# Performance work log

Measured on AMD Instinct MI355X. Metric: run time of the kernel, lower is better.

Reference implementation:

```python
import jax, jax.numpy as jnp
import numpy as np

N_NODES = 100000
FIELD_DIM = 128
EMBED_DIM = 64
N_EDGES = 3200000
BATCH = 8192
NUM_FIELDS = 2


def setup_inputs() -> dict:
    key = jax.random.key(0)
    k1, k2, k3, k4 = jax.random.split(key, 4)
    features = jax.random.normal(k1, (N_NODES, FIELD_DIM), dtype=jnp.float32)
    edge_index = jax.random.randint(k2, (2, N_EDGES), 0, N_NODES, dtype=jnp.int32)
    # GCNConv linear weight (Glorot-ish scale) and bias
    W = jax.random.normal(k3, (FIELD_DIM, EMBED_DIM), dtype=jnp.float32) * (1.0 / np.sqrt(FIELD_DIM))
    bias = jnp.zeros((EMBED_DIM,), dtype=jnp.float32)
    x = jax.random.randint(k4, (BATCH, NUM_FIELDS), 0, N_NODES, dtype=jnp.int32)
    return {"features": features, "edge_index": edge_index, "W": W, "bias": bias, "x": x}


def reference(features, edge_index, W, bias, x):
    # GCNConv: out = D^{-1/2} (A + I) D^{-1/2} (X W) + b, then gather rows by x.
    n = features.shape[0]
    loop = jnp.arange(n, dtype=edge_index.dtype)
    src = jnp.concatenate([edge_index[0], loop])  # [E + N]
    dst = jnp.concatenate([edge_index[1], loop])  # [E + N]
    # degree (with self-loops) per destination node; >= 1 so rsqrt is safe
    deg = jax.ops.segment_sum(jnp.ones_like(dst, dtype=features.dtype), dst, num_segments=n)
    dinv = jax.lax.rsqrt(deg)
    norm = dinv[src] * dinv[dst]  # [E + N]
    h = features @ W  # [N, EMBED_DIM]
    msgs = h[src] * norm[:, None]  # gather + scale
    out = jax.ops.segment_sum(msgs, dst, num_segments=n) + bias  # [N, EMBED_DIM]
    return out[x]  # [BATCH, NUM_FIELDS, EMBED_DIM]
```

## Files before the change

### kernel.cpp

```cpp
#include <hip/hip_runtime.h>

#define N_NODES   100000
#define FIELD_DIM 128
#define EMBED_DIM 64
#define N_EDGES   3200000
#define NX        16384

#define NRANGE    2
#define RN        50000
#define RNH       25000
#define NSLICE    125
#define SLICE_E   (N_EDGES / NSLICE)
#define HISTB     (NRANGE * NSLICE)
#define SB_N      16384
#define EXB       (N_EDGES / 1024)
#define GEMMB     ((N_NODES + 63) / 64)
#define EGB       (EXB + GEMMB)
#define PCAP      5120

typedef short  bf16x8 __attribute__((ext_vector_type(8)));
typedef float  f32x4  __attribute__((ext_vector_type(4)));

__device__ __forceinline__ unsigned short f2bf(float x) {
    unsigned u = __float_as_uint(x);
    u += 0x7FFF + ((u >> 16) & 1);
    return (unsigned short)(u >> 16);
}
__device__ __forceinline__ float bf2f(unsigned short b) {
    return __uint_as_float(((unsigned)b) << 16);
}
__device__ __forceinline__ unsigned pk2(float lo, float hi) {
    return (unsigned)f2bf(lo) | ((unsigned)f2bf(hi) << 16);
}

__global__ __launch_bounds__(1024) void k_histzero(const int* __restrict__ dst,
                                                   unsigned int* __restrict__ partial32,
                                                   float4* __restrict__ z4) {
    int tid = threadIdx.x;
    if (blockIdx.x == HISTB) {
        for (int i = tid; i < 1284; i += 1024) z4[i] = make_float4(0.f, 0.f, 0.f, 0.f);
        return;
    }
    __shared__ unsigned int hist[RNH];
    int q = blockIdx.x & 1, s = blockIdx.x >> 1;
    for (int i = tid; i < RNH; i += 1024) hist[i] = 0;
    __syncthreads();
    int lo = q * RN;
    const int4* dp = (const int4*)(dst + s * SLICE_E);
    for (int i = tid; i < SLICE_E / 4; i += 1024) {
        int4 d = dp[i];
        int a;
        a = d.x - lo; if ((unsigned)a < RN) atomicAdd(&hist[a >> 1], 1u << ((a & 1) << 4));
        a = d.y - lo; if ((unsigned)a < RN) atomicAdd(&hist[a >> 1], 1u << ((a & 1) << 4));
        a = d.z - lo; if ((unsigned)a < RN) atomicAdd(&hist[a >> 1], 1u << ((a & 1) << 4));
        a = d.w - lo; if ((unsigned)a < RN) atomicAdd(&hist[a >> 1], 1u << ((a & 1) << 4));
    }
    __syncthreads();
    unsigned int* po = partial32 + (size_t)blockIdx.x * RNH;
    for (int i = tid; i < RNH; i += 1024) po[i] = hist[i];
}

__global__ void k_init(const int* __restrict__ x, unsigned int* __restrict__ bits,
                       const float* __restrict__ W, unsigned short* __restrict__ Wt) {
    int b = blockIdx.x;
    if (b < 64) {
        int i = b * 256 + threadIdx.x;
        int v = x[i];
        atomicOr(&bits[v >> 5], 1u << (v & 31));
    } else {
        for (int o = threadIdx.x; o < FIELD_DIM * EMBED_DIM; o += 256) {
            int c = o >> 7, k = o & 127;
            Wt[o] = f2bf(W[k * EMBED_DIM + c]);
        }
    }
}

__global__ __launch_bounds__(256) void k_reduce(const unsigned int* __restrict__ partial32,
                                                const unsigned int* __restrict__ bits,
                                                int* __restrict__ cnt,
                                                float* __restrict__ dinv,
                                                int* __restrict__ nlist,
                                                int* __restrict__ inv,
                                                int* __restrict__ off,
                                                int* __restrict__ sbase_t,
                                                unsigned long long* __restrict__ counters) {
    __shared__ int wtot[4], wedge[4], ptot[4], pedge[4];
    __shared__ unsigned int baseN, baseE;
    int tid = threadIdx.x;
    int v = blockIdx.x * 256 + tid;
    bool inb = (v < N_NODES);
    int vc = inb ? v : (N_NODES - 1);
    int q = vc / RN, loc = vc - q * RN;
    int i2 = loc >> 1, sh = (loc & 1) << 4;
    const unsigned int* p = partial32 + (size_t)q * RNH + i2;
    unsigned short vals[NSLICE];
#pragma unroll
    for (int s = 0; s < NSLICE; ++s)
        vals[s] = (unsigned short)((p[(size_t)s * (NRANGE * RNH)] >> sh) & 0xFFFFu);
    int c = 0;
#pragma unroll
    for (int s = 0; s < NSLICE; ++s) c += vals[s];
    if (inb) {
        cnt[v] = c;
        dinv[v] = rsqrtf((float)c + 1.0f);
    }
    bool fl = inb && ((bits[v >> 5] >> (v & 31)) & 1u);
    int lane = tid & 63;
    int w = tid >> 6;
    unsigned long long mask = __ballot(fl);
    int cc = fl ? c : 0;
    int incl = cc;
#pragma unroll
    for (int o = 1; o < 64; o <<= 1) {
        int t = __shfl_up(incl, o);
        if (lane >= o) incl += t;
    }
    if (lane == 63) { wtot[w] = __popcll(mask); wedge[w] = incl; }
    int myi = __popcll(mask & ((1ull << lane) - 1));
    int excl = incl - cc;
    __syncthreads();
    if (tid == 0) {
        int t0 = wtot[0], t1 = wtot[1], t2 = wtot[2], t3 = wtot[3];
        int e0 = wedge[0], e1 = wedge[1], e2 = wedge[2], e3 = wedge[3];
        ptot[0] = 0; ptot[1] = t0; ptot[2] = t0 + t1; ptot[3] = t0 + t1 + t2;
        pedge[0] = 0; pedge[1] = e0; pedge[2] = e0 + e1; pedge[3] = e0 + e1 + e2;
        int bt = t0 + t1 + t2 + t3;
        int be = e0 + e1 + e2 + e3;
        if (bt > 0) {
            unsigned long long add = ((unsigned long long)(unsigned)be << 32) |
                                     (unsigned long long)(unsigned)bt;
            unsigned long long old = atomicAdd(counters, add);
            baseN = (unsigned)(old & 0xFFFFFFFFull);
            baseE = (unsigned)(old >> 32);
        } else {
            baseN = 0; baseE = 0;
        }
    }
    __syncthreads();
    if (fl) {
        int ic = (int)baseN + ptot[w] + myi;
        int oc = (int)baseE + pedge[w] + excl;
        nlist[ic] = v;
        inv[v] = ic;
        off[v] = oc;
        int cum = 0;
#pragma unroll
        for (int s = 0; s < NSLICE; ++s) {
            sbase_t[(size_t)s * SB_N + ic] = oc + cum;
            cum += vals[s];
        }
    }
}

__global__ __launch_bounds__(256) void k_exgemm(const int* __restrict__ src,
                                                const int* __restrict__ dst,
                                                const unsigned int* __restrict__ bits,
                                                const int* __restrict__ inv,
                                                int2* __restrict__ pairs,
                                                int* __restrict__ scur16,
                                                const float* __restrict__ F,
                                                const unsigned short* __restrict__ Wt,
                                                unsigned short* __restrict__ h) {
    int bk = blockIdx.x;
    int tid = threadIdx.x;
    bool isg = ((bk % 3) == 0) && (bk / 3 < GEMMB);
    if (!isg) {
        __shared__ int wsum[4];
        __shared__ int sbase;
        int b = bk - min(bk / 3 + 1, GEMMB);
        int lane = tid & 63, w = tid >> 6;
        int slice = b / 25;
        const int4* dp = (const int4*)(dst + b * 1024);
        const int4* sp = (const int4*)(src + b * 1024);
        int4 d4 = dp[tid];
        int4 s4 = sp[tid];
        int dd[4] = {d4.x, d4.y, d4.z, d4.w};
        int ss[4] = {s4.x, s4.y, s4.z, s4.w};
        bool fl[4];
        int nf = 0;
#pragma unroll
        for (int u = 0; u < 4; ++u) {
            fl[u] = (bits[(unsigned)dd[u] >> 5] >> (dd[u] & 31)) & 1u;
            nf += fl[u] ? 1 : 0;
        }
        int incl = nf;
#pragma unroll
        for (int o = 1; o < 64; o <<= 1) {
            int t = __shfl_up(incl, o);
            if (lane >= o) incl += t;
        }
        if (lane == 63) wsum[w] = incl;
        __syncthreads();
        if (tid == 0) {
            int bt = wsum[0] + wsum[1] + wsum[2] + wsum[3];
            sbase = bt ? atomicAdd(&scur16[slice * 16], bt) : 0;
        }
        __syncthreads();
        int wbase = (w > 0 ? wsum[0] : 0) + (w > 1 ? wsum[1] : 0) + (w > 2 ? wsum[2] : 0);
        int pos = sbase + wbase + incl - nf;
        int2* po = pairs + (size_t)slice * PCAP;
#pragma unroll
        for (int u = 0; u < 4; ++u) {
            if (fl[u]) {
                if (pos < PCAP) po[pos] = make_int2(inv[dd[u]], ss[u]);
                ++pos;
            }
        }
        return;
    }
    int gb = bk / 3;
    int wave = tid >> 6, lane = tid & 63;
    int l15 = lane & 15, kg = lane >> 4;

    const char* wb = (const char*)Wt;
    bf16x8 bfrag[4][4];
#pragma unroll
    for (int cb = 0; cb < 4; ++cb)
#pragma unroll
        for (int ks = 0; ks < 4; ++ks)
            bfrag[cb][ks] = *(const bf16x8*)(wb + (cb * 16 + l15) * 256 + ks * 64 + kg * 16);

    int row = gb * 64 + wave * 16 + l15;
    int rowc = min(row, N_NODES - 1);
    const float4* F4 = (const float4*)(F + (size_t)rowc * FIELD_DIM + kg * 8);

    f32x4 acc[4];
#pragma unroll
    for (int cb = 0; cb < 4; ++cb) acc[cb] = (f32x4){0.f, 0.f, 0.f, 0.f};

#pragma unroll
    for (int ks = 0; ks < 4; ++ks) {
        float4 fa = F4[ks * 8];
        float4 fb = F4[ks * 8 + 1];
        union { bf16x8 v; unsigned u[4]; } af;
        af.u[0] = pk2(fa.x, fa.y);
        af.u[1] = pk2(fa.z, fa.w);
        af.u[2] = pk2(fb.x, fb.y);
        af.u[3] = pk2(fb.z, fb.w);
#pragma unroll
        for (int cb = 0; cb < 4; ++cb)
            acc[cb] = __builtin_amdgcn_mfma_f32_16x16x32_bf16(af.v, bfrag[cb][ks],
                                                              acc[cb], 0, 0, 0);
    }
    int rbase = gb * 64 + wave * 16 + kg * 4;
#pragma unroll
    for (int r = 0; r < 4; ++r) {
        int orow = rbase + r;
        if (orow < N_NODES) {
            unsigned short* hp = h + (size_t)orow * 64 + l15;
#pragma unroll
            for (int cb = 0; cb < 4; ++cb) hp[cb * 16] = f2bf(acc[cb][r]);
        }
    }
}

__global__ __launch_bounds__(1024) void k_place(const int2* __restrict__ pairs,
                                                const int* __restrict__ scur16,
                                                const int* __restrict__ sbase_t,
                                                int* __restrict__ elist) {
    __shared__ int cur[SB_N];
    int s = blockIdx.x, tid = threadIdx.x;
    const int* srow = sbase_t + (size_t)s * SB_N;
    for (int i = tid; i < SB_N; i += 1024) cur[i] = srow[i];
    __syncthreads();
    int tot = min(scur16[s * 16], PCAP);
    const int2* pp = pairs + (size_t)s * PCAP;
    for (int r = tid; r < tot; r += 1024) {
        int2 p = pp[r];
        int slot = atomicAdd(&cur[p.x], 1);
        elist[slot] = p.y;
    }
}

__global__ __launch_bounds__(256) void k_pull(const int* __restrict__ nlist,
                                              const int* __restrict__ counters,
                                              const int* __restrict__ cnt,
                                              const int* __restrict__ off,
                                              const int* __restrict__ elist,
                                              const unsigned short* __restrict__ h,
                                              const float* __restrict__ dinv,
                                              const float* __restrict__ bias,
                                              float* __restrict__ accc) {
    int t = blockIdx.x * blockDim.x + threadIdx.x;
    int wid = t >> 6;
    int lane = t & 63;
    if (wid >= counters[0]) return;
    int v = nlist[wid];
    float dvd = dinv[v];
    int deg = cnt[v];
    int base = off[v];
    float acc = bf2f(h[(size_t)v * 64 + lane]) * (dvd * dvd) + bias[lane];
    float acc2 = 0.f;
    int j = 0;
    for (; j + 7 < deg; j += 8) {
        int s0 = elist[base + j + 0];
        int s1 = elist[base + j + 1];
        int s2 = elist[base + j + 2];
        int s3 = elist[base + j + 3];
        int s4 = elist[base + j + 4];
        int s5 = elist[base + j + 5];
        int s6 = elist[base + j + 6];
        int s7 = elist[base + j + 7];
        float v0 = bf2f(h[(size_t)s0 * 64 + lane]);
        float v1 = bf2f(h[(size_t)s1 * 64 + lane]);
        float v2 = bf2f(h[(size_t)s2 * 64 + lane]);
        float v3 = bf2f(h[(size_t)s3 * 64 + lane]);
        float v4 = bf2f(h[(size_t)s4 * 64 + lane]);
        float v5 = bf2f(h[(size_t)s5 * 64 + lane]);
        float v6 = bf2f(h[(size_t)s6 * 64 + lane]);
        float v7 = bf2f(h[(size_t)s7 * 64 + lane]);
        float n0 = dinv[s0], n1 = dinv[s1], n2 = dinv[s2], n3 = dinv[s3];
        float n4 = dinv[s4], n5 = dinv[s5], n6 = dinv[s6], n7 = dinv[s7];
        acc  += v0 * (n0 * dvd);
        acc2 += v1 * (n1 * dvd);
        acc  += v2 * (n2 * dvd);
        acc2 += v3 * (n3 * dvd);
        acc  += v4 * (n4 * dvd);
        acc2 += v5 * (n5 * dvd);
        acc  += v6 * (n6 * dvd);
        acc2 += v7 * (n7 * dvd);
    }
    for (; j < deg; ++j) {
        int s0 = elist[base + j];
        acc += bf2f(h[(size_t)s0 * 64 + lane]) * (dinv[s0] * dvd);
    }
    accc[(size_t)wid * 64 + lane] = acc + acc2;
}

__global__ void k_gather(const int* __restrict__ x,
                         const int* __restrict__ inv,
                         const float* __restrict__ accc,
                         float* __restrict__ out) {
    int g = blockIdx.x * blockDim.x + threadIdx.x;
    if (g >= NX * 64) return;
    int v = x[g >> 6];
    out[g] = accc[(size_t)inv[v] * 64 + (g & 63)];
}

extern "C" void kernel_launch(void* const* d_in, const int* in_sizes, int n_in,
                              void* d_out, int out_size, void* d_ws, size_t ws_size,
                              hipStream_t stream) {
    const float* features = (const float*)d_in[0];
    const int*   edge     = (const int*)d_in[1];
    const float* W        = (const float*)d_in[2];
    const float* bias     = (const float*)d_in[3];
    const int*   x        = (const int*)d_in[4];
    float* out = (float*)d_out;

    char* ws = (char*)d_ws;
    unsigned short* h16      = (unsigned short*)(ws);
    int*            elist    = (int*)(ws + 12800000);
    unsigned int*   partial32= (unsigned int*)(ws + 16800000);
    int2*           pairs    = (int2*)(ws + 16800000);
    float*          accc     = (float*)(ws + 21920000);
    int*            sbase_t  = (int*)  (ws + 41800000);
    int*            cnt      = (int*)  (ws + 49992000);
    float*          dinv     = (float*)(ws + 50392000);
    int*            off      = (int*)  (ws + 50792000);
    int*            inv      = (int*)  (ws + 51192000);
    int*            nlist    = (int*)  (ws + 51592000);
    int*            scur16   = (int*)  (ws + 51657536);
    unsigned long long* counters = (unsigned long long*)(ws + 51665536);
    unsigned int*   bits     = (unsigned int*) (ws + 51665568);
    unsigned short* Wt       = (unsigned short*)(ws + 51678080);

    const int* esrc = edge;
    const int* edst = edge + N_EDGES;

    k_histzero<<<HISTB + 1, 1024, 0, stream>>>(edst, partial32,
                                               (float4*)(ws + 51657536));
    k_init    <<<65, 256, 0, stream>>>(x, bits, W, Wt);
    k_reduce  <<<(N_NODES + 255) / 256, 256, 0, stream>>>(partial32, bits, cnt, dinv,
                                                          nlist, inv, off, sbase_t, counters);
    k_exgemm  <<<EGB, 256, 0, stream>>>(esrc, edst, bits, inv, pairs, scur16,
                                        features, Wt, h16);
    k_place   <<<NSLICE, 1024, 0, stream>>>(pairs, scur16, sbase_t, elist);
    k_pull    <<<(NX * 64 + 255) / 256, 256, 0, stream>>>(nlist, (const int*)counters,
                                                          cnt, off, elist, h16, dinv,
                                                          bias, accc);
    k_gather  <<<(NX * 64 + 255) / 256, 256, 0, stream>>>(x, inv, accc, out);
}
```

Baseline: 102.1 us.

## Split each node's neighbor pull across two wavefronts and merge init into histogram kernel

k_pull now gives each destination node two wavefronts, each summing half of the neighbor list, and combines the two partial sums through shared memory. This doubles the parallelism available to hide gather latency, at the cost of more blocks and a block-wide barrier. Separately, the bitmap and transposed-weight setup work from k_init moves into extra blocks of the histogram kernel. A tiny k_zero kernel now clears the counters, which previously happened in an extra histogram block.

```diff
diff --git a/kernel.cpp b/kernel.cpp
--- a/kernel.cpp
+++ b/kernel.cpp
@@ -12,6 +12,7 @@
 #define NSLICE    125
 #define SLICE_E   (N_EDGES / NSLICE)
 #define HISTB     (NRANGE * NSLICE)
+#define HIB       (HISTB + 17)
 #define SB_N      16384
 #define EXB       (N_EDGES / 1024)
 #define GEMMB     ((N_NODES + 63) / 64)
@@ -33,16 +34,34 @@
     return (unsigned)f2bf(lo) | ((unsigned)f2bf(hi) << 16);
 }
 
-__global__ __launch_bounds__(1024) void k_histzero(const int* __restrict__ dst,
+__global__ void k_zero(float4* __restrict__ z4) {
+    int i = blockIdx.x * blockDim.x + threadIdx.x;
+    if (i < 1284) z4[i] = make_float4(0.f, 0.f, 0.f, 0.f);
+}
+
+__global__ __launch_bounds__(1024) void k_histinit(const int* __restrict__ dst,
                                                    unsigned int* __restrict__ partial32,
-                                                   float4* __restrict__ z4) {
+                                                   const int* __restrict__ x,
+                                                   unsigned int* __restrict__ bits,
+                                                   const float* __restrict__ W,
+                                                   unsigned short* __restrict__ Wt) {
     int tid = threadIdx.x;
-    if (blockIdx.x == HISTB) {
-        for (int i = tid; i < 1284; i += 1024) z4[i] = make_float4(0.f, 0.f, 0.f, 0.f);
+    int b = blockIdx.x;
+    if (b >= HISTB) {
+        if (b < HISTB + 16) {
+            int i = (b - HISTB) * 1024 + tid;
+            int v = x[i];
+            atomicOr(&bits[v >> 5], 1u << (v & 31));
+        } else {
+            for (int o = tid; o < FIELD_DIM * EMBED_DIM; o += 1024) {
+                int c = o >> 7, k = o & 127;
+                Wt[o] = f2bf(W[k * EMBED_DIM + c]);
+            }
+        }
         return;
     }
     __shared__ unsigned int hist[RNH];
-    int q = blockIdx.x & 1, s = blockIdx.x >> 1;
+    int q = b & 1, s = b >> 1;
     for (int i = tid; i < RNH; i += 1024) hist[i] = 0;
     __syncthreads();
     int lo = q * RN;
@@ -56,23 +75,8 @@
         a = d.w - lo; if ((unsigned)a < RN) atomicAdd(&hist[a >> 1], 1u << ((a & 1) << 4));
     }
     __syncthreads();
-    unsigned int* po = partial32 + (size_t)blockIdx.x * RNH;
+    unsigned int* po = partial32 + (size_t)b * RNH;
     for (int i = tid; i < RNH; i += 1024) po[i] = hist[i];
-}
-
-__global__ void k_init(const int* __restrict__ x, unsigned int* __restrict__ bits,
-                       const float* __restrict__ W, unsigned short* __restrict__ Wt) {
-    int b = blockIdx.x;
-    if (b < 64) {
-        int i = b * 256 + threadIdx.x;
-        int v = x[i];
-        atomicOr(&bits[v >> 5], 1u << (v & 31));
-    } else {
-        for (int o = threadIdx.x; o < FIELD_DIM * EMBED_DIM; o += 256) {
-            int c = o >> 7, k = o & 127;
-            Wt[o] = f2bf(W[k * EMBED_DIM + c]);
-        }
-    }
 }
 
 __global__ __launch_bounds__(256) void k_reduce(const unsigned int* __restrict__ partial32,
@@ -281,18 +285,25 @@
                                               const float* __restrict__ dinv,
                                               const float* __restrict__ bias,
                                               float* __restrict__ accc) {
-    int t = blockIdx.x * blockDim.x + threadIdx.x;
-    int wid = t >> 6;
-    int lane = t & 63;
-    if (wid >= counters[0]) return;
-    int v = nlist[wid];
+    __shared__ float part[2][64];
+    int tid = threadIdx.x;
+    int w = tid >> 6, lane = tid & 63;
+    int pairi = w >> 1, half = w & 1;
+    int node = blockIdx.x * 2 + pairi;
+    int nflag = counters[0];
+    bool valid = (node < nflag);
+    int vc = valid ? node : 0;
+    int v = nlist[vc];
     float dvd = dinv[v];
     int deg = cnt[v];
     int base = off[v];
-    float acc = bf2f(h[(size_t)v * 64 + lane]) * (dvd * dvd) + bias[lane];
-    float acc2 = 0.f;
-    int j = 0;
-    for (; j + 7 < deg; j += 8) {
+    int d0 = (deg >> 1) & ~7;
+    int jb = half ? d0 : 0;
+    int je = half ? deg : d0;
+    float acc = 0.f, acc2 = 0.f;
+    if (half) acc = bf2f(h[(size_t)v * 64 + lane]) * (dvd * dvd) + bias[lane];
+    int j = jb;
+    for (; j + 7 < je; j += 8) {
         int s0 = elist[base + j + 0];
         int s1 = elist[base + j + 1];
         int s2 = elist[base + j + 2];
@@ -320,11 +331,14 @@
         acc  += v6 * (n6 * dvd);
         acc2 += v7 * (n7 * dvd);
     }
-    for (; j < deg; ++j) {
+    for (; j < je; ++j) {
         int s0 = elist[base + j];
         acc += bf2f(h[(size_t)s0 * 64 + lane]) * (dinv[s0] * dvd);
     }
-    accc[(size_t)wid * 64 + lane] = acc + acc2;
+    if (half) part[pairi][lane] = acc + acc2;
+    __syncthreads();
+    if (!half && valid)
+        accc[(size_t)node * 64 + lane] = acc + acc2 + part[pairi][lane];
 }
 
 __global__ void k_gather(const int* __restrict__ x,
@@ -367,16 +381,15 @@
     const int* esrc = edge;
     const int* edst = edge + N_EDGES;
 
-    k_histzero<<<HISTB + 1, 1024, 0, stream>>>(edst, partial32,
-                                               (float4*)(ws + 51657536));
-    k_init    <<<65, 256, 0, stream>>>(x, bits, W, Wt);
+    k_zero    <<<6, 256, 0, stream>>>((float4*)(ws + 51657536));
+    k_histinit<<<HIB, 1024, 0, stream>>>(edst, partial32, x, bits, W, Wt);
     k_reduce  <<<(N_NODES + 255) / 256, 256, 0, stream>>>(partial32, bits, cnt, dinv,
                                                           nlist, inv, off, sbase_t, counters);
     k_exgemm  <<<EGB, 256, 0, stream>>>(esrc, edst, bits, inv, pairs, scur16,
                                         features, Wt, h16);
     k_place   <<<NSLICE, 1024, 0, stream>>>(pairs, scur16, sbase_t, elist);
-    k_pull    <<<(NX * 64 + 255) / 256, 256, 0, stream>>>(nlist, (const int*)counters,
-                                                          cnt, off, elist, h16, dinv,
-                                                          bias, accc);
+    k_pull    <<<(2 * NX + 1) / 2, 256, 0, stream>>>(nlist, (const int*)counters,
+                                                     cnt, off, elist, h16, dinv,
+                                                     bias, accc);
     k_gather  <<<(NX * 64 + 255) / 256, 256, 0, stream>>>(x, inv, accc, out);
 }
```

Result: slower. 120.3 us (+17.8%).
